# Kernel optimization log

Measured on AMD Instinct MI355X. Metric: run time of the kernel, lower is better.

Reference implementation:

```python
import jax, jax.numpy as jnp
import numpy as np

BS = 16
CIN = 32          # input_channels
COUT = 64         # out_channels
OUT_DIM = 1024    # out_dim
S = 2
S0 = 1
K = S * (S0 + 1)  # non-overlapping patch size = 4
D = OUT_DIM * K   # input spatial length = 4096


def setup_inputs() -> dict:
    key = jax.random.key(0)
    k1, k2 = jax.random.split(key)
    x = jax.random.normal(k1, (BS, CIN, D), dtype=jnp.float32)
    # learned parameter, torch.randn init
    weight = jax.random.normal(k2, (COUT, CIN, D), dtype=jnp.float32)
    return {"x": x, "weight": weight}


def reference(x, weight):
    # sharing == 0 path of NonOverlappingLocallyConnected1d:
    #   out[b,o,p] = (1/sqrt(CIN)) * sum_{c,k} x[b,c,p*K+k] * weight[o,c,p*K+k]
    # Original materializes [bs,cout,cin,D] via broadcast multiply then sums
    # over (cin, K); fused here as a single einsum over non-overlapping patches.
    bs = x.shape[0]
    xr = x.reshape(bs, CIN, OUT_DIM, K)        # [b, c, p, k]
    wr = weight.reshape(COUT, CIN, OUT_DIM, K)  # [o, c, p, k]
    out = jnp.einsum('bcpk,ocpk->bop', xr, wr)  # [b, o, p]
    return out / jnp.sqrt(jnp.asarray(CIN, x.dtype))
```

## Files before the change

kernel.cpp:

```cpp
#include <hip/hip_runtime.h>

#define CIN     32
#define COUT    64
#define OUT_DIM 1024
#define RS4     1024

__global__ __launch_bounds__(512, 2) void nolc1d_kernel(
    const float* __restrict__ x,
    const float* __restrict__ w,
    float* __restrict__ out)
{
    const int bid = blockIdx.x;
    const int xcd = bid & 7;
    const int m   = bid >> 3;
    const int og  = m & 3;
    const int pc  = xcd * 8 + (m >> 2);
    const int o0  = og * 16;
    const int pf0 = pc * 16;

    const int t    = threadIdx.x;
    const int lane = t & 63;
    const int wv   = t >> 6;
    const int p    = t & 15;
    const int cs   = (t >> 4) & 1;
    const int g    = (t >> 5) & 3;
    const int oq   = t >> 7;

    __shared__ float4 wls[2][2048];
    __shared__ float4 xls[2][2048];

    const float4* __restrict__ x4 = (const float4*)x;
    const float4* __restrict__ w4 = (const float4*)w;

    const int r4 = lane >> 4;
    const int q  = lane & 15;

    auto stage = [&](int buf, int ci) {
        #pragma unroll
        for (int i = 0; i < 4; ++i) {
            const int s   = wv * 4 + i;
            const int row = s * 4 + r4;
            const int hi  = row >> 3;
            const int c   = ci * 8 + (row & 7);
            const float4* srcw =
                &w4[((o0 + hi) * CIN + c) * RS4 + pf0 + q];
            __builtin_amdgcn_global_load_lds(
                (const __attribute__((address_space(1))) void*)srcw,
                (__attribute__((address_space(3))) void*)&wls[buf][s * 64],
                16, 0, 0);
            const float4* srcx =
                &x4[(hi * CIN + c) * RS4 + pf0 + q];
            __builtin_amdgcn_global_load_lds(
                (const __attribute__((address_space(1))) void*)srcx,
                (__attribute__((address_space(3))) void*)&xls[buf][s * 64],
                16, 0, 0);
        }
    };

    float acc[4][4] = {};

    stage(0, 0);
    __syncthreads();

    #pragma unroll 1
    for (int ci = 0; ci < 4; ++ci) {
        if (ci < 3) stage((ci + 1) & 1, ci + 1);
        const int buf = ci & 1;
        #pragma unroll
        for (int jj = 0; jj < 4; ++jj) {
            const int cl = cs * 4 + jj;
            float4 xv[4], wq[4];
            #pragma unroll
            for (int bi = 0; bi < 4; ++bi)
                xv[bi] = xls[buf][((g * 4 + bi) * 8 + cl) * 16 + p];
            #pragma unroll
            for (int oi = 0; oi < 4; ++oi)
                wq[oi] = wls[buf][((oq * 4 + oi) * 8 + cl) * 16 + p];
            #pragma unroll
            for (int bi = 0; bi < 4; ++bi)
                #pragma unroll
                for (int oi = 0; oi < 4; ++oi)
                    acc[bi][oi] += xv[bi].x * wq[oi].x + xv[bi].y * wq[oi].y +
                                   xv[bi].z * wq[oi].z + xv[bi].w * wq[oi].w;
        }
        if (ci < 3) __syncthreads();
    }

    #pragma unroll
    for (int bi = 0; bi < 4; ++bi)
        #pragma unroll
        for (int oi = 0; oi < 4; ++oi)
            acc[bi][oi] += __shfl_xor(acc[bi][oi], 16, 64);

    const float scale = 0.17677669529663687f;
    if (cs == 0) {
        #pragma unroll
        for (int bi = 0; bi < 4; ++bi)
            #pragma unroll
            for (int oi = 0; oi < 4; ++oi)
                out[((size_t)(4 * g + bi) * COUT + o0 + 4 * oq + oi) * OUT_DIM
                    + pf0 + p] = acc[bi][oi] * scale;
    }
}

extern "C" void kernel_launch(void* const* d_in, const int* in_sizes, int n_in,
                              void* d_out, int out_size, void* d_ws, size_t ws_size,
                              hipStream_t stream) {
    const float* x = (const float*)d_in[0];
    const float* w = (const float*)d_in[1];
    float* out = (float*)d_out;

    nolc1d_kernel<<<dim3(256), dim3(512), 0, stream>>>(x, w, out);
}
```

Before: 83.63 us.

## Halve patch tile per block, double grid, and pipeline eight channel stages

Each block now covers 8 patch float4s instead of 16, so the grid doubles to 512 blocks. The channel loop becomes 8 stages of 4 channels, each a single global_load_lds per thread. LDS per block drops fourfold, and launch bounds now request 4 blocks per CU to raise occupancy and latency hiding on a memory-bound kernel. In exchange, each load row is 128 bytes instead of 256, there are more barriers, and the cross-channel reduction needs an extra shuffle.

```diff
diff --git a/kernel.cpp b/kernel.cpp
--- a/kernel.cpp
+++ b/kernel.cpp
@@ -5,7 +5,7 @@
 #define OUT_DIM 1024
 #define RS4     1024
 
-__global__ __launch_bounds__(512, 2) void nolc1d_kernel(
+__global__ __launch_bounds__(512, 4) void nolc1d_kernel(
     const float* __restrict__ x,
     const float* __restrict__ w,
     float* __restrict__ out)
@@ -14,47 +14,42 @@
     const int xcd = bid & 7;
     const int m   = bid >> 3;
     const int og  = m & 3;
-    const int pc  = xcd * 8 + (m >> 2);
+    const int pc  = xcd * 16 + (m >> 2);
     const int o0  = og * 16;
-    const int pf0 = pc * 16;
+    const int pf0 = pc * 8;
 
     const int t    = threadIdx.x;
     const int lane = t & 63;
     const int wv   = t >> 6;
-    const int p    = t & 15;
-    const int cs   = (t >> 4) & 1;
+    const int p    = t & 7;
+    const int cs   = (t >> 3) & 3;
     const int g    = (t >> 5) & 3;
     const int oq   = t >> 7;
 
-    __shared__ float4 wls[2][2048];
-    __shared__ float4 xls[2][2048];
+    __shared__ float4 wls[2][512];
+    __shared__ float4 xls[2][512];
 
     const float4* __restrict__ x4 = (const float4*)x;
     const float4* __restrict__ w4 = (const float4*)w;
 
-    const int r4 = lane >> 4;
-    const int q  = lane & 15;
-
+    const int srow = wv * 8 + (lane >> 3);
+    const int shi  = srow >> 2;
+    const int scl  = srow & 3;
+    const int sq   = lane & 7;
     auto stage = [&](int buf, int ci) {
-        #pragma unroll
-        for (int i = 0; i < 4; ++i) {
-            const int s   = wv * 4 + i;
-            const int row = s * 4 + r4;
-            const int hi  = row >> 3;
-            const int c   = ci * 8 + (row & 7);
-            const float4* srcw =
-                &w4[((o0 + hi) * CIN + c) * RS4 + pf0 + q];
-            __builtin_amdgcn_global_load_lds(
-                (const __attribute__((address_space(1))) void*)srcw,
-                (__attribute__((address_space(3))) void*)&wls[buf][s * 64],
-                16, 0, 0);
-            const float4* srcx =
-                &x4[(hi * CIN + c) * RS4 + pf0 + q];
-            __builtin_amdgcn_global_load_lds(
-                (const __attribute__((address_space(1))) void*)srcx,
-                (__attribute__((address_space(3))) void*)&xls[buf][s * 64],
-                16, 0, 0);
-        }
+        const int c = ci * 4 + scl;
+        const float4* srcw =
+            &w4[((o0 + shi) * CIN + c) * RS4 + pf0 + sq];
+        __builtin_amdgcn_global_load_lds(
+            (const __attribute__((address_space(1))) void*)srcw,
+            (__attribute__((address_space(3))) void*)&wls[buf][wv * 64],
+            16, 0, 0);
+        const float4* srcx =
+            &x4[(shi * CIN + c) * RS4 + pf0 + sq];
+        __builtin_amdgcn_global_load_lds(
+            (const __attribute__((address_space(1))) void*)srcx,
+            (__attribute__((address_space(3))) void*)&xls[buf][wv * 64],
+            16, 0, 0);
     };
 
     float acc[4][4] = {};
@@ -63,34 +58,32 @@
     __syncthreads();
 
     #pragma unroll 1
-    for (int ci = 0; ci < 4; ++ci) {
-        if (ci < 3) stage((ci + 1) & 1, ci + 1);
+    for (int ci = 0; ci < 8; ++ci) {
+        if (ci < 7) stage((ci + 1) & 1, ci + 1);
         const int buf = ci & 1;
+        float4 xv[4], wq[4];
         #pragma unroll
-        for (int jj = 0; jj < 4; ++jj) {
-            const int cl = cs * 4 + jj;
-            float4 xv[4], wq[4];
-            #pragma unroll
-            for (int bi = 0; bi < 4; ++bi)
-                xv[bi] = xls[buf][((g * 4 + bi) * 8 + cl) * 16 + p];
+        for (int bi = 0; bi < 4; ++bi)
+            xv[bi] = xls[buf][((g * 4 + bi) * 4 + cs) * 8 + p];
+        #pragma unroll
+        for (int oi = 0; oi < 4; ++oi)
+            wq[oi] = wls[buf][((oq * 4 + oi) * 4 + cs) * 8 + p];
+        #pragma unroll
+        for (int bi = 0; bi < 4; ++bi)
             #pragma unroll
             for (int oi = 0; oi < 4; ++oi)
-                wq[oi] = wls[buf][((oq * 4 + oi) * 8 + cl) * 16 + p];
-            #pragma unroll
-            for (int bi = 0; bi < 4; ++bi)
-                #pragma unroll
-                for (int oi = 0; oi < 4; ++oi)
-                    acc[bi][oi] += xv[bi].x * wq[oi].x + xv[bi].y * wq[oi].y +
-                                   xv[bi].z * wq[oi].z + xv[bi].w * wq[oi].w;
-        }
-        if (ci < 3) __syncthreads();
+                acc[bi][oi] += xv[bi].x * wq[oi].x + xv[bi].y * wq[oi].y +
+                               xv[bi].z * wq[oi].z + xv[bi].w * wq[oi].w;
+        if (ci < 7) __syncthreads();
     }
 
     #pragma unroll
     for (int bi = 0; bi < 4; ++bi)
         #pragma unroll
-        for (int oi = 0; oi < 4; ++oi)
+        for (int oi = 0; oi < 4; ++oi) {
+            acc[bi][oi] += __shfl_xor(acc[bi][oi], 8, 64);
             acc[bi][oi] += __shfl_xor(acc[bi][oi], 16, 64);
+        }
 
     const float scale = 0.17677669529663687f;
     if (cs == 0) {
@@ -99,7 +92,7 @@
             #pragma unroll
             for (int oi = 0; oi < 4; ++oi)
                 out[((size_t)(4 * g + bi) * COUT + o0 + 4 * oq + oi) * OUT_DIM
-                    + pf0 + p] = acc[bi][oi] * scale;
+                    + pc * 8 + p] = acc[bi][oi] * scale;
     }
 }
 
@@ -110,5 +103,5 @@
     const float* w = (const float*)d_in[1];
     float* out = (float*)d_out;
 
-    nolc1d_kernel<<<dim3(256), dim3(512), 0, stream>>>(x, w, out);
+    nolc1d_kernel<<<dim3(512), dim3(512), 0, stream>>>(x, w, out);
 }
```

New measurement: 84.26 us. No clear change (+0.8%).
